# Optimization experiments

Hardware: AMD Instinct MI355X
Metric: run time of the kernel (lower is better)

The kernel has to match this reference:

```python
import jax, jax.numpy as jnp
import numpy as np

N_NODES = 50000
BN_EPS = 1e-5


def _gin_layer(x, src, dst, W1, b1, gamma, beta, W2, b2):
    # GINConv (eps=0): h = MLP(x + sum_{j->i} x_j)
    agg = jax.ops.segment_sum(x[src], dst, num_segments=N_NODES)  # [N, F]
    h = (x + agg) @ W1 + b1                                       # [N, H]
    # BatchNorm1d over node dim (training-mode batch statistics, biased var)
    mean = jnp.mean(h, axis=0)
    var = jnp.mean((h - mean) ** 2, axis=0)
    h = (h - mean) * jax.lax.rsqrt(var + BN_EPS) * gamma + beta
    h = jax.nn.relu(h)
    h = jax.nn.relu(h @ W2 + b2)
    return h


def setup_inputs() -> dict:
    key = jax.random.key(0)
    ks = jax.random.split(key, 16)
    F_in, H = 9, 256
    E = 800000
    x = jax.random.normal(ks[0], (N_NODES, F_in), dtype=jnp.float32)
    edge_index = jax.random.randint(ks[1], (2, E), 0, N_NODES, dtype=jnp.int64)

    def lin(k, fi, fo):
        s = 1.0 / np.sqrt(fi)
        kw, kb = jax.random.split(k)
        W = jax.random.uniform(kw, (fi, fo), jnp.float32, -s, s)
        b = jax.random.uniform(kb, (fo,), jnp.float32, -s, s)
        return W, b

    inp = {"x": x, "edge_index": edge_index}
    dims = [(F_in, H), (H, H), (H, H)]
    for i, (fi, fo) in enumerate(dims, start=1):
        W1, b1 = lin(ks[2 * i], fi, fo)
        W2, b2 = lin(ks[2 * i + 1], fo, fo)
        inp[f"W1_{i}"] = W1; inp[f"b1_{i}"] = b1
        inp[f"g_{i}"] = jnp.ones((fo,), jnp.float32)
        inp[f"be_{i}"] = jnp.zeros((fo,), jnp.float32)
        inp[f"W2_{i}"] = W2; inp[f"b2_{i}"] = b2
    return inp


def reference(x, edge_index,
              W1_1, b1_1, g_1, be_1, W2_1, b2_1,
              W1_2, b1_2, g_2, be_2, W2_2, b2_2,
              W1_3, b1_3, g_3, be_3, W2_3, b2_3):
    src, dst = edge_index[0], edge_index[1]
    h = _gin_layer(x, src, dst, W1_1, b1_1, g_1, be_1, W2_1, b2_1)
    h = jax.nn.relu(h)
    h = _gin_layer(h, src, dst, W1_2, b1_2, g_2, be_2, W2_2, b2_2)
    h = jax.nn.relu(h)
    h = _gin_layer(h, src, dst, W1_3, b1_3, g_3, be_3, W2_3, b2_3)
    h = jax.nn.relu(h)
    return jnp.sum(h, axis=0)  # [256]
```

## Files before the change

### kernel.cpp

```cpp
#include <hip/hip_runtime.h>

#define NN 50000
#define NE 800000
#define HD 256
#define BN_EPS 1e-5f

typedef __attribute__((ext_vector_type(8))) short bf16x8;
typedef __attribute__((ext_vector_type(8))) unsigned short ushort8;
typedef __attribute__((ext_vector_type(4))) float f32x4;

__device__ __forceinline__ float bf2f(unsigned short u) {
  union { unsigned int i; float f; } c; c.i = ((unsigned int)u) << 16; return c.f;
}
__device__ __forceinline__ unsigned short f2bf(float x) {
  union { float f; unsigned int i; } c; c.f = x;
  unsigned int r = (c.i + 0x7fffu + ((c.i >> 16) & 1u)) >> 16;
  return (unsigned short)r;
}

__global__ __launch_bounds__(1024) void k_zero(int* __restrict__ cursor, float* __restrict__ s_sum,
                                               float* __restrict__ s_sq, float* __restrict__ out) {
  int i = blockIdx.x * 1024 + threadIdx.x;
  if (i < NN) cursor[i] = 0;
  if (i < HD) { s_sum[i] = 0.f; s_sq[i] = 0.f; out[i] = 0.f; }
}

__global__ __launch_bounds__(256) void k_count(const int* __restrict__ dst, int* __restrict__ cnt) {
  int e = blockIdx.x * 256 + threadIdx.x;
  if (e < NE) atomicAdd(&cnt[dst[e]], 1);
}

__global__ __launch_bounds__(1024) void k_scan_a(const int* __restrict__ cnt,
                                                 int* __restrict__ rp, int* __restrict__ bsum) {
  __shared__ int wsum[16];
  int i = blockIdx.x * 1024 + threadIdx.x;
  int v = (i < NN) ? cnt[i] : 0;
  int lane = threadIdx.x & 63, wid = threadIdx.x >> 6;
  int s = v;
  #pragma unroll
  for (int off = 1; off < 64; off <<= 1) {
    int tv = __shfl_up(s, off);
    if (lane >= off) s += tv;
  }
  if (lane == 63) wsum[wid] = s;
  __syncthreads();
  if (wid == 0) {
    int ws = (lane < 16) ? wsum[lane] : 0;
    #pragma unroll
    for (int off = 1; off < 16; off <<= 1) {
      int tv = __shfl_up(ws, off);
      if (lane >= off) ws += tv;
    }
    if (lane < 16) wsum[lane] = ws;
  }
  __syncthreads();
  int excl = s - v + (wid > 0 ? wsum[wid - 1] : 0);
  if (i < NN) rp[i] = excl;
  if (threadIdx.x == 1023) bsum[blockIdx.x] = excl + v;
}

__global__ __launch_bounds__(1024) void k_scan_b(const int* __restrict__ bsum,
                                                 int* __restrict__ rp, int* __restrict__ cursor) {
  __shared__ int off_s;
  if (threadIdx.x < 64) {
    int v = ((int)threadIdx.x < (int)blockIdx.x && threadIdx.x < 49) ? bsum[threadIdx.x] : 0;
    #pragma unroll
    for (int o = 32; o > 0; o >>= 1) v += __shfl_xor(v, o);
    if (threadIdx.x == 0) off_s = v;
  }
  __syncthreads();
  int i = blockIdx.x * 1024 + threadIdx.x;
  if (i < NN) {
    int r = rp[i] + off_s;
    rp[i] = r;
    cursor[i] = r;
  }
  if (blockIdx.x == 0 && threadIdx.x == 0) rp[NN] = NE;
}

__global__ __launch_bounds__(256) void k_fill(const int* __restrict__ src, const int* __restrict__ dst,
                                              int* __restrict__ cursor, int* __restrict__ col) {
  int e = blockIdx.x * 256 + threadIdx.x;
  if (e < NE) {
    int p = atomicAdd(&cursor[dst[e]], 1);
    col[p] = src[e];
  }
}

__global__ __launch_bounds__(256) void k_prepW5(const float* __restrict__ Wa, const float* __restrict__ Wb,
    const float* __restrict__ Wc, const float* __restrict__ Wd, const float* __restrict__ We,
    unsigned short* __restrict__ out) {
  const float* W = (blockIdx.y == 0) ? Wa : (blockIdx.y == 1) ? Wb : (blockIdx.y == 2) ? Wc
                   : (blockIdx.y == 3) ? Wd : We;
  unsigned short* O = out + (size_t)blockIdx.y * HD * HD;
  int k = blockIdx.x, n = threadIdx.x;
  int nt = n >> 4, ks = k >> 5, lane = ((k >> 3) & 3) * 16 + (n & 15), j = k & 7;
  O[(size_t)((nt * 8 + ks) * 64 + lane) * 8 + j] = f2bf(W[k * 256 + n]);
}

__global__ __launch_bounds__(256) void k_agg9(const float* __restrict__ x,
    const int* __restrict__ rp, const int* __restrict__ col, float* __restrict__ u) {
  int i = blockIdx.x * 256 + threadIdx.x;
  if (i >= NN) return;
  float a[9];
  #pragma unroll
  for (int k = 0; k < 9; ++k) a[k] = x[(size_t)i * 9 + k];
  int e1 = rp[i + 1];
  for (int e = rp[i]; e < e1; ++e) {
    int nb = col[e];
    #pragma unroll
    for (int k = 0; k < 9; ++k) a[k] += x[(size_t)nb * 9 + k];
  }
  #pragma unroll
  for (int k = 0; k < 9; ++k) u[(size_t)i * 16 + k] = a[k];
}

__global__ __launch_bounds__(256) void k_l1gemm(const float* __restrict__ u,
    const float* __restrict__ W1, const float* __restrict__ b1,
    unsigned short* __restrict__ h, float* __restrict__ s_sum, float* __restrict__ s_sq) {
  __shared__ float Ws[9][256];
  int t = threadIdx.x;
  #pragma unroll
  for (int k = 0; k < 9; ++k) Ws[k][t] = W1[k * 256 + t];
  float bj = b1[t];
  __syncthreads();
  int r0 = blockIdx.x * 128;
  int r1 = min(r0 + 128, NN);
  float sum = 0.f, sq = 0.f;
  for (int r = r0; r < r1; ++r) {
    float acc = bj;
    #pragma unroll
    for (int k = 0; k < 9; ++k) acc = fmaf(u[(size_t)r * 16 + k], Ws[k][t], acc);
    h[(size_t)r * 256 + t] = f2bf(acc);
    sum += acc; sq += acc * acc;
  }
  atomicAdd(&s_sum[t], sum);
  atomicAdd(&s_sq[t], sq);
}

__global__ void k_finalize(float* __restrict__ s_sum, float* __restrict__ s_sq,
                           const float* __restrict__ g, const float* __restrict__ be,
                           float* __restrict__ scale, float* __restrict__ shift) {
  int j = threadIdx.x;
  float m = s_sum[j] / (float)NN;
  float v = s_sq[j] / (float)NN - m * m;
  v = fmaxf(v, 0.f);
  float sc = rsqrtf(v + BN_EPS) * g[j];
  scale[j] = sc;
  shift[j] = be[j] - m * sc;
  s_sum[j] = 0.f;
  s_sq[j] = 0.f;
}

__global__ __launch_bounds__(256) void k_agg256(const unsigned short* __restrict__ f,
    const int* __restrict__ rp, const int* __restrict__ col, unsigned short* __restrict__ u) {
  int half = threadIdx.x >> 5;
  int lane32 = threadIdx.x & 31;
  int node = blockIdx.x * 8 + threadIdx.y * 2 + half;
  if (node >= NN) return;
  float acc[8];
  ushort8 v = *(const ushort8*)(f + (size_t)node * HD + lane32 * 8);
  #pragma unroll
  for (int j = 0; j < 8; ++j) acc[j] = bf2f(v[j]);
  int e0 = rp[node], e1 = rp[node + 1];
  int e = e0;
  for (; e + 3 < e1; e += 4) {
    int nb0 = col[e], nb1 = col[e + 1], nb2 = col[e + 2], nb3 = col[e + 3];
    ushort8 w0 = *(const ushort8*)(f + (size_t)nb0 * HD + lane32 * 8);
    ushort8 w1 = *(const ushort8*)(f + (size_t)nb1 * HD + lane32 * 8);
    ushort8 w2 = *(const ushort8*)(f + (size_t)nb2 * HD + lane32 * 8);
    ushort8 w3 = *(const ushort8*)(f + (size_t)nb3 * HD + lane32 * 8);
    #pragma unroll
    for (int j = 0; j < 8; ++j)
      acc[j] += (bf2f(w0[j]) + bf2f(w1[j])) + (bf2f(w2[j]) + bf2f(w3[j]));
  }
  for (; e < e1; ++e) {
    int nb = col[e];
    ushort8 w = *(const ushort8*)(f + (size_t)nb * HD + lane32 * 8);
    #pragma unroll
    for (int j = 0; j < 8; ++j) acc[j] += bf2f(w[j]);
  }
  ushort8 o;
  #pragma unroll
  for (int j = 0; j < 8; ++j) o[j] = f2bf(acc[j]);
  *(ushort8*)(u + (size_t)node * HD + lane32 * 8) = o;
}

template<bool PRE_BN, bool STATS, bool RELU, bool OUTSUM, bool WRITE>
__global__ __launch_bounds__(256, 2) void k_mfma_gemm(
    const unsigned short* __restrict__ A, const unsigned short* __restrict__ Bp,
    const float* __restrict__ bias, const float* __restrict__ scale, const float* __restrict__ shift,
    unsigned short* __restrict__ C,
    float* __restrict__ s_sum, float* __restrict__ s_sq, float* __restrict__ out)
{
  __shared__ unsigned short As[4][64 * 64];
  __shared__ float scLds[256], shLds[256];
  const int t = threadIdx.x;
  const int w = t >> 6;
  const int lane = t & 63;
  const int brow = blockIdx.x * 64;
  const bf16x8* Bf = (const bf16x8*)Bp;

  if (PRE_BN) { scLds[t] = scale[t]; shLds[t] = shift[t]; }

  #pragma unroll
  for (int tt = 0; tt < 4; ++tt) {
    #pragma unroll
    for (int hh = 0; hh < 2; ++hh) {
      int r0 = w * 16 + hh * 8;
      int row = r0 + (lane >> 3);
      int gp = (lane & 7) ^ (row & 7);
      int grow = brow + row; if (grow >= NN) grow = NN - 1;
      const unsigned short* gptr = A + (size_t)grow * HD + tt * 64 + gp * 8;
      __builtin_amdgcn_global_load_lds(
          (const __attribute__((address_space(1))) void*)gptr,
          (__attribute__((address_space(3))) void*)&As[tt][r0 * 64], 16, 0, 0);
    }
  }

  bf16x8 bfr[3][4];
  #pragma unroll
  for (int p = 0; p < 3; ++p)
    #pragma unroll
    for (int ntl = 0; ntl < 4; ++ntl)
      bfr[p][ntl] = Bf[(size_t)((w * 4 + ntl) * 8 + p) * 64 + lane];

  f32x4 zero; zero.x = zero.y = zero.z = zero.w = 0.f;
  f32x4 acc[4][4];
  #pragma unroll
  for (int i = 0; i < 4; ++i)
    #pragma unroll
    for (int j = 0; j < 4; ++j) acc[i][j] = zero;

  #pragma unroll
  for (int step = 0; step < 8; ++step) {
    const int tt = step >> 1, s = step & 1;
    if (s == 0) __syncthreads();
    const int cur = step % 3;
    float scv[8], shv[8];
    if (PRE_BN) {
      int kb = tt * 64 + s * 32 + (lane >> 4) * 8;
      #pragma unroll
      for (int j = 0; j < 8; ++j) { scv[j] = scLds[kb + j]; shv[j] = shLds[kb + j]; }
    }
    bf16x8 afr[4];
    #pragma unroll
    for (int mt = 0; mt < 4; ++mt) {
      int row = mt * 16 + (lane & 15);
      int g = s * 4 + (lane >> 4);
      int gp = g ^ (row & 7);
      afr[mt] = *(const bf16x8*)&As[tt][row * 64 + gp * 8];
      if (PRE_BN) {
        bf16x8 a = afr[mt];
        bf16x8 o;
        #pragma unroll
        for (int j = 0; j < 8; ++j) {
          float v = bf2f((unsigned short)a[j]);
          v = fmaxf(fmaf(v, scv[j], shv[j]), 0.f);
          o[j] = (short)f2bf(v);
        }
        afr[mt] = o;
      }
    }
    #pragma unroll
    for (int mt = 0; mt < 4; ++mt)
      #pragma unroll
      for (int ntl = 0; ntl < 4; ++ntl)
        acc[mt][ntl] = __builtin_amdgcn_mfma_f32_16x16x32_bf16(
            afr[mt], bfr[cur][ntl], acc[mt][ntl], 0, 0, 0);
    if (step < 5) {
      #pragma unroll
      for (int ntl = 0; ntl < 4; ++ntl)
        bfr[cur][ntl] = Bf[(size_t)((w * 4 + ntl) * 8 + step + 3) * 64 + lane];
    }
  }

  const int cl = lane & 15;
  const int rq = (lane >> 4) * 4;
  #pragma unroll
  for (int ntl = 0; ntl < 4; ++ntl) {
    const int cgl = w * 64 + ntl * 16 + cl;
    const float bv = bias[cgl];
    float s = 0.f, q = 0.f;
    #pragma unroll
    for (int mt = 0; mt < 4; ++mt) {
      #pragma unroll
      for (int i = 0; i < 4; ++i) {
        float v = acc[mt][ntl][i] + bv;
        if (RELU) v = fmaxf(v, 0.f);
        int grow = brow + mt * 16 + rq + i;
        bool valid = grow < NN;
        if (WRITE && valid) C[(size_t)grow * HD + cgl] = f2bf(v);
        if ((STATS || OUTSUM) && valid) { s += v; if (STATS) q += v * v; }
      }
    }
    if (STATS || OUTSUM) {
      s += __shfl_xor(s, 16); s += __shfl_xor(s, 32);
      if (STATS) { q += __shfl_xor(q, 16); q += __shfl_xor(q, 32); }
      if (lane < 16) {
        if (STATS) { atomicAdd(&s_sum[cgl], s); atomicAdd(&s_sq[cgl], q); }
        if (OUTSUM) atomicAdd(&out[cgl], s);
      }
    }
  }
}

extern "C" void kernel_launch(void* const* d_in, const int* in_sizes, int n_in,
                              void* d_out, int out_size, void* d_ws, size_t ws_size,
                              hipStream_t stream) {
  (void)in_sizes; (void)n_in; (void)out_size; (void)ws_size;
  const float* x  = (const float*)d_in[0];
  const int*  ei  = (const int*)d_in[1];
  const int*  src = ei;
  const int*  dst = ei + NE;
  const float* W1[3] = {(const float*)d_in[2],  (const float*)d_in[8],  (const float*)d_in[14]};
  const float* b1[3] = {(const float*)d_in[3],  (const float*)d_in[9],  (const float*)d_in[15]};
  const float* g_[3] = {(const float*)d_in[4],  (const float*)d_in[10], (const float*)d_in[16]};
  const float* be[3] = {(const float*)d_in[5],  (const float*)d_in[11], (const float*)d_in[17]};
  const float* W2[3] = {(const float*)d_in[6],  (const float*)d_in[12], (const float*)d_in[18]};
  const float* b2[3] = {(const float*)d_in[7],  (const float*)d_in[13], (const float*)d_in[19]};

  char* ws = (char*)d_ws;
  size_t o = 0;
  auto alloc = [&](size_t bytes) -> void* {
    void* p = ws + o;
    o += (bytes + 255) & ~(size_t)255;
    return p;
  };
  int*   rp     = (int*)alloc((size_t)(NN + 1) * 4);
  int*   cursor = (int*)alloc((size_t)NN * 4);
  int*   col    = (int*)alloc((size_t)NE * 4);
  int*   bsum   = (int*)alloc(64 * 4);
  float* u9     = (float*)alloc((size_t)NN * 16 * 4);
  unsigned short* ubf = (unsigned short*)alloc((size_t)NN * HD * 2);
  unsigned short* hbf = (unsigned short*)alloc((size_t)NN * HD * 2);
  unsigned short* fbf = (unsigned short*)alloc((size_t)NN * HD * 2);
  unsigned short* Wp  = (unsigned short*)alloc((size_t)5 * HD * HD * 2);
  float* s_sum  = (float*)alloc(HD * 4);
  float* s_sq   = (float*)alloc(HD * 4);
  float* scale  = (float*)alloc(HD * 4);
  float* shift  = (float*)alloc(HD * 4);
  float* out    = (float*)d_out;

  const int SCB = (NN + 1023) / 1024;

  k_zero<<<SCB, 1024, 0, stream>>>(cursor, s_sum, s_sq, out);
  k_count<<<(NE + 255) / 256, 256, 0, stream>>>(dst, cursor);
  k_scan_a<<<SCB, 1024, 0, stream>>>(cursor, rp, bsum);
  k_scan_b<<<SCB, 1024, 0, stream>>>(bsum, rp, cursor);
  k_fill<<<(NE + 255) / 256, 256, 0, stream>>>(src, dst, cursor, col);
  k_prepW5<<<dim3(256, 5), 256, 0, stream>>>(W2[0], W1[1], W2[1], W1[2], W2[2], Wp);

  unsigned short* WpA[5];
  for (int i = 0; i < 5; ++i) WpA[i] = Wp + (size_t)i * HD * HD;

  const int gemmGrid = (NN + 63) / 64;
  dim3 aGrid((NN + 7) / 8);
  dim3 aBlk(64, 4);

  k_agg9<<<(NN + 255) / 256, 256, 0, stream>>>(x, rp, col, u9);
  k_l1gemm<<<(NN + 127) / 128, 256, 0, stream>>>(u9, W1[0], b1[0], hbf, s_sum, s_sq);
  k_finalize<<<1, HD, 0, stream>>>(s_sum, s_sq, g_[0], be[0], scale, shift);
  k_mfma_gemm<true, false, true, false, true><<<gemmGrid, 256, 0, stream>>>(
      hbf, WpA[0], b2[0], scale, shift, fbf, nullptr, nullptr, nullptr);

  k_agg256<<<aGrid, aBlk, 0, stream>>>(fbf, rp, col, ubf);
  k_mfma_gemm<false, true, false, false, true><<<gemmGrid, 256, 0, stream>>>(
      ubf, WpA[1], b1[1], nullptr, nullptr, hbf, s_sum, s_sq, nullptr);
  k_finalize<<<1, HD, 0, stream>>>(s_sum, s_sq, g_[1], be[1], scale, shift);
  k_mfma_gemm<true, false, true, false, true><<<gemmGrid, 256, 0, stream>>>(
      hbf, WpA[2], b2[1], scale, shift, fbf, nullptr, nullptr, nullptr);

  k_agg256<<<aGrid, aBlk, 0, stream>>>(fbf, rp, col, ubf);
  k_mfma_gemm<false, true, false, false, true><<<gemmGrid, 256, 0, stream>>>(
      ubf, WpA[3], b1[2], nullptr, nullptr, hbf, s_sum, s_sq, nullptr);
  k_finalize<<<1, HD, 0, stream>>>(s_sum, s_sq, g_[2], be[2], scale, shift);
  k_mfma_gemm<true, false, true, true, false><<<gemmGrid, 256, 0, stream>>>(
      hbf, WpA[4], b2[2], scale, shift, nullptr, nullptr, nullptr, out);
}
```

Baseline: 480.6 us.

## Remap 256-wide aggregation to four threads per node looping over column chunks

The neighbor-sum kernel previously gave each node 32 lanes, each loading one 16-byte slice of every neighbor row. It now gives each node 4 threads, so a wavefront covers 16 nodes and walks 8 column chunks of 32 features each. The aim is to cut per-edge index-load redundancy and spread warp divergence from uneven degrees across more nodes. The cost is that each wavefront load instruction now touches 16 scattered 64-byte segments instead of two full 512-byte rows, and the edge list is re-read 8 times per node, which may hurt memory coalescing.

```diff
diff --git a/kernel.cpp b/kernel.cpp
--- a/kernel.cpp
+++ b/kernel.cpp
@@ -152,38 +152,44 @@
   s_sq[j] = 0.f;
 }
 
-__global__ __launch_bounds__(256) void k_agg256(const unsigned short* __restrict__ f,
+__global__ __launch_bounds__(256) void k_agg256p(const unsigned short* __restrict__ f,
     const int* __restrict__ rp, const int* __restrict__ col, unsigned short* __restrict__ u) {
-  int half = threadIdx.x >> 5;
-  int lane32 = threadIdx.x & 31;
-  int node = blockIdx.x * 8 + threadIdx.y * 2 + half;
+  int grp = threadIdx.x >> 2;
+  int sub = threadIdx.x & 3;
+  int node = blockIdx.x * 64 + grp;
   if (node >= NN) return;
-  float acc[8];
-  ushort8 v = *(const ushort8*)(f + (size_t)node * HD + lane32 * 8);
-  #pragma unroll
-  for (int j = 0; j < 8; ++j) acc[j] = bf2f(v[j]);
-  int e0 = rp[node], e1 = rp[node + 1];
-  int e = e0;
-  for (; e + 3 < e1; e += 4) {
-    int nb0 = col[e], nb1 = col[e + 1], nb2 = col[e + 2], nb3 = col[e + 3];
-    ushort8 w0 = *(const ushort8*)(f + (size_t)nb0 * HD + lane32 * 8);
-    ushort8 w1 = *(const ushort8*)(f + (size_t)nb1 * HD + lane32 * 8);
-    ushort8 w2 = *(const ushort8*)(f + (size_t)nb2 * HD + lane32 * 8);
-    ushort8 w3 = *(const ushort8*)(f + (size_t)nb3 * HD + lane32 * 8);
-    #pragma unroll
-    for (int j = 0; j < 8; ++j)
-      acc[j] += (bf2f(w0[j]) + bf2f(w1[j])) + (bf2f(w2[j]) + bf2f(w3[j]));
-  }
-  for (; e < e1; ++e) {
-    int nb = col[e];
-    ushort8 w = *(const ushort8*)(f + (size_t)nb * HD + lane32 * 8);
-    #pragma unroll
-    for (int j = 0; j < 8; ++j) acc[j] += bf2f(w[j]);
-  }
-  ushort8 o;
-  #pragma unroll
-  for (int j = 0; j < 8; ++j) o[j] = f2bf(acc[j]);
-  *(ushort8*)(u + (size_t)node * HD + lane32 * 8) = o;
+  const int e0 = rp[node], e1 = rp[node + 1];
+  const size_t nodeOff = (size_t)node * HD;
+  #pragma unroll 1
+  for (int c = 0; c < 8; ++c) {
+    const int c0 = c * 32 + sub * 8;
+    const unsigned short* fp = f + c0;
+    float acc[8];
+    ushort8 v = *(const ushort8*)(fp + nodeOff);
+    #pragma unroll
+    for (int j = 0; j < 8; ++j) acc[j] = bf2f(v[j]);
+    int e = e0;
+    for (; e + 3 < e1; e += 4) {
+      int nb0 = col[e], nb1 = col[e + 1], nb2 = col[e + 2], nb3 = col[e + 3];
+      ushort8 w0 = *(const ushort8*)(fp + (size_t)nb0 * HD);
+      ushort8 w1 = *(const ushort8*)(fp + (size_t)nb1 * HD);
+      ushort8 w2 = *(const ushort8*)(fp + (size_t)nb2 * HD);
+      ushort8 w3 = *(const ushort8*)(fp + (size_t)nb3 * HD);
+      #pragma unroll
+      for (int j = 0; j < 8; ++j)
+        acc[j] += (bf2f(w0[j]) + bf2f(w1[j])) + (bf2f(w2[j]) + bf2f(w3[j]));
+    }
+    for (; e < e1; ++e) {
+      int nb = col[e];
+      ushort8 w = *(const ushort8*)(fp + (size_t)nb * HD);
+      #pragma unroll
+      for (int j = 0; j < 8; ++j) acc[j] += bf2f(w[j]);
+    }
+    ushort8 o;
+    #pragma unroll
+    for (int j = 0; j < 8; ++j) o[j] = f2bf(acc[j]);
+    *(ushort8*)(u + nodeOff + c0) = o;
+  }
 }
 
 template<bool PRE_BN, bool STATS, bool RELU, bool OUTSUM, bool WRITE>
@@ -355,8 +361,7 @@
   for (int i = 0; i < 5; ++i) WpA[i] = Wp + (size_t)i * HD * HD;
 
   const int gemmGrid = (NN + 63) / 64;
-  dim3 aGrid((NN + 7) / 8);
-  dim3 aBlk(64, 4);
+  const int aggGrid = (NN + 63) / 64;
 
   k_agg9<<<(NN + 255) / 256, 256, 0, stream>>>(x, rp, col, u9);
   k_l1gemm<<<(NN + 127) / 128, 256, 0, stream>>>(u9, W1[0], b1[0], hbf, s_sum, s_sq);
@@ -364,14 +369,14 @@
   k_mfma_gemm<true, false, true, false, true><<<gemmGrid, 256, 0, stream>>>(
       hbf, WpA[0], b2[0], scale, shift, fbf, nullptr, nullptr, nullptr);
 
-  k_agg256<<<aGrid, aBlk, 0, stream>>>(fbf, rp, col, ubf);
+  k_agg256p<<<aggGrid, 256, 0, stream>>>(fbf, rp, col, ubf);
   k_mfma_gemm<false, true, false, false, true><<<gemmGrid, 256, 0, stream>>>(
       ubf, WpA[1], b1[1], nullptr, nullptr, hbf, s_sum, s_sq, nullptr);
   k_finalize<<<1, HD, 0, stream>>>(s_sum, s_sq, g_[1], be[1], scale, shift);
   k_mfma_gemm<true, false, true, false, true><<<gemmGrid, 256, 0, stream>>>(
       hbf, WpA[2], b2[1], scale, shift, fbf, nullptr, nullptr, nullptr);
 
-  k_agg256<<<aGrid, aBlk, 0, stream>>>(fbf, rp, col, ubf);
+  k_agg256p<<<aggGrid, 256, 0, stream>>>(fbf, rp, col, ubf);
   k_mfma_gemm<false, true, false, false, true><<<gemmGrid, 256, 0, stream>>>(
       ubf, WpA[3], b1[2], nullptr, nullptr, hbf, s_sum, s_sq, nullptr);
   k_finalize<<<1, HD, 0, stream>>>(s_sum, s_sq, g_[2], be[2], scale, shift);
```

After: 545.7 us. 13.5% more time.
